# Kernel tuning notes

Hardware: AMD Instinct MI355X
Metric: run time of the kernel (lower is better)

Reference implementation:

```python
import jax, jax.numpy as jnp
import numpy as np

B, L, P, T, D, H = 16, 50, 49, 20, 512, 8
DH = D // H
DFF = 4 * D
EPS = 1e-6
NEG = -1000000000.0


def gelu_tanh(x):
    return 0.5 * x * (1.0 + jnp.tanh(jnp.sqrt(2.0 / jnp.pi) * (x + 0.044715 * x ** 3)))


def layernorm(x, a, b):
    # torch LayerNorm (custom): unbiased std, divide by (std + eps)
    mean = jnp.mean(x, axis=-1, keepdims=True)
    std = jnp.sqrt(jnp.var(x, axis=-1, keepdims=True, ddof=1))
    return a * (x - mean) / (std + EPS) + b


def setup_inputs() -> dict:
    key = jax.random.key(0)
    ks = jax.random.split(key, 20)
    s = 0.02
    return {
        "img": jax.random.normal(ks[0], (B, L, P, D), jnp.float32),
        "title": jax.random.normal(ks[1], (B, L, T, D), jnp.float32),
        "mask": jax.random.randint(ks[2], (B, L, T), 0, 2, jnp.int32),
        "scale_img": jax.random.normal(ks[3], (H, P), jnp.float32) * 0.1,
        "scale_title": jax.random.normal(ks[4], (H, T), jnp.float32) * 0.1,
        "w_proj": jax.random.normal(ks[5], (D, D), jnp.float32) * s,
        "b_proj": jnp.zeros((D,), jnp.float32),
        "w1_img": jax.random.normal(ks[6], (DFF, D), jnp.float32) * s,
        "b1_img": jnp.zeros((DFF,), jnp.float32),
        "w2_img": jax.random.normal(ks[7], (D, DFF), jnp.float32) * s,
        "b2_img": jnp.zeros((D,), jnp.float32),
        "w1_tit": jax.random.normal(ks[8], (DFF, D), jnp.float32) * s,
        "b1_tit": jnp.zeros((DFF,), jnp.float32),
        "w2_tit": jax.random.normal(ks[9], (D, DFF), jnp.float32) * s,
        "b2_tit": jnp.zeros((D,), jnp.float32),
        "ln_a_img": jnp.ones((D,), jnp.float32),
        "ln_b_img": jnp.zeros((D,), jnp.float32),
        "ln_a_tit": jnp.ones((D,), jnp.float32),
        "ln_b_tit": jnp.zeros((D,), jnp.float32),
    }


def _forward(img, title, mask, scale_img, scale_title, w_proj, b_proj,
             w1_img, b1_img, w2_img, b2_img, w1_tit, b1_tit, w2_tit, b2_tit,
             ln_a_img, ln_b_img, ln_a_tit, ln_b_tit):
    imgh = img.reshape(B, L, P, H, DH)      # [B,L,P,H,dh]
    tith = title.reshape(B, L, T, H, DH)    # [B,L,T,H,dh]

    raw = jnp.einsum('blphd,blthd->blhpt', imgh, tith) / jnp.sqrt(jnp.float32(DH))
    # corr_title is the transpose of the UNSCALED corr_img
    corr_img = raw * scale_img[None, None, :, :, None]                     # [B,L,H,P,T]
    corr_tit = jnp.swapaxes(raw, -1, -2) * scale_title[None, None, :, :, None]  # [B,L,H,T,P]

    m_img = mask[:, :, None, None, :]  # [B,L,1,1,T] -> broadcast over H,P
    m_tit = mask[:, :, None, :, None]  # [B,L,1,T,1]
    corr_img = jnp.where(m_img == 0, NEG, corr_img)
    corr_tit = jnp.where(m_tit == 0, NEG, corr_tit)

    p_img = jax.nn.softmax(corr_img, axis=-1)  # [B,L,H,P,T]
    p_tit = jax.nn.softmax(corr_tit, axis=-1)  # [B,L,H,T,P]

    # T != P, so the torch code takes the else branch (swapped outputs)
    hid_img = jnp.einsum('blhtp,blphd->blthd', p_tit, imgh).reshape(B, L, T, D)
    hid_tit = jnp.einsum('blhpt,blthd->blphd', p_img, tith).reshape(B, L, P, D)

    # both projected with img_layer (faithful to source)
    hid_img = hid_img @ w_proj.T + b_proj
    hid_tit = hid_tit @ w_proj.T + b_proj

    ffn_img = gelu_tanh(hid_img @ w1_img.T + b1_img) @ w2_img.T + b2_img
    ffn_tit = gelu_tanh(hid_tit @ w1_tit.T + b1_tit) @ w2_tit.T + b2_tit

    out_img = hid_img + layernorm(ffn_img, ln_a_img, ln_b_img)
    out_tit = hid_tit + layernorm(ffn_tit, ln_a_tit, ln_b_tit)
    return out_img, out_tit


def reference(img, title, mask, scale_img, scale_title, w_proj, b_proj,
              w1_img, b1_img, w2_img, b2_img, w1_tit, b1_tit, w2_tit, b2_tit,
              ln_a_img, ln_b_img, ln_a_tit, ln_b_tit):
    return _forward(img, title, mask, scale_img, scale_title, w_proj, b_proj,
                    w1_img, b1_img, w2_img, b2_img, w1_tit, b1_tit, w2_tit, b2_tit,
                    ln_a_img, ln_b_img, ln_a_tit, ln_b_tit)
```

## Files before the change

### kernel.cpp

```cpp
#include <hip/hip_runtime.h>
#include <hip/hip_bf16.h>

#define BB   16
#define LL   50
#define PP   49
#define TT   20
#define DD   512
#define HH   8
#define DHH  64
#define DFF  2048

#define BL     (BB*LL)
#define ROWS_I (BL*TT)
#define ROWS_T (BL*PP)
#define ROWS_A (ROWS_I+ROWS_T)
#define OUT_I_ELEMS ((size_t)ROWS_I*DD)
#define CHUNK 19600

#define R1_OFF 80281600ull
#define R2_OFF 136806400ull
#define R3_OFF 176947200ull

typedef __attribute__((ext_vector_type(8))) short bf16x8;
typedef __attribute__((ext_vector_type(4))) float f32x4;

__device__ __forceinline__ unsigned short f2bf(float f) {
    union { float f; unsigned int i; } w; w.f = f;
    unsigned int x = w.i;
    unsigned int r = (x + 0x7fffu + ((x >> 16) & 1u)) >> 16;
    return (unsigned short)r;
}
__device__ __forceinline__ float gelu_tanh_f(float x) {
    float c = 0.7978845608028654f * (x + 0.044715f * x * x * x);
    return 0.5f * x * (1.0f + tanhf(c));
}

__global__ __launch_bounds__(256) void cvt_kernel(
    const float* __restrict__ s, unsigned short* __restrict__ d, int n4)
{
    int i = blockIdx.x * 256 + threadIdx.x;
    if (i < n4) {
        float4 v = ((const float4*)s)[i];
        ushort4 u;
        u.x = f2bf(v.x); u.y = f2bf(v.y); u.z = f2bf(v.z); u.w = f2bf(v.w);
        ((ushort4*)d)[i] = u;
    }
}

__global__ __launch_bounds__(256) void attn_kernel(
    const float* __restrict__ img, const float* __restrict__ title,
    const int* __restrict__ mask, const float* __restrict__ scale_img,
    const float* __restrict__ scale_tit, unsigned short* __restrict__ hid)
{
    const int blh = blockIdx.x;
    const int h  = blh & 7;
    const int bl = blh >> 3;
    const int tid = threadIdx.x;

    __shared__ float simg[PP][DHH + 1];
    __shared__ float stit[TT][DHH + 1];
    __shared__ float S [PP][TT];
    __shared__ float pI[PP][TT];
    __shared__ float pT[TT][PP];
    __shared__ int   msk[TT];

    const float* imgbase = img   + (size_t)bl * PP * DD + h * DHH;
    const float* titbase = title + (size_t)bl * TT * DD + h * DHH;
    for (int i = tid; i < PP * DHH; i += 256) {
        int p = i >> 6, d = i & 63;
        simg[p][d] = imgbase[(size_t)p * DD + d];
    }
    for (int i = tid; i < TT * DHH; i += 256) {
        int t = i >> 6, d = i & 63;
        stit[t][d] = titbase[(size_t)t * DD + d];
    }
    if (tid < TT) msk[tid] = mask[bl * TT + tid];
    __syncthreads();

    for (int i = tid; i < PP * TT; i += 256) {
        int p = i / TT, t = i % TT;
        float s = 0.f;
        #pragma unroll 8
        for (int d = 0; d < DHH; ++d) s += simg[p][d] * stit[t][d];
        S[p][t] = s * 0.125f;
    }
    __syncthreads();

    if (tid < PP) {
        const int p = tid;
        const float sc = scale_img[h * PP + p];
        float m = -1e30f;
        #pragma unroll
        for (int t = 0; t < TT; ++t) {
            float x = (msk[t] == 0) ? -1e9f : S[p][t] * sc;
            m = fmaxf(m, x);
        }
        float sum = 0.f;
        #pragma unroll
        for (int t = 0; t < TT; ++t) {
            float x = (msk[t] == 0) ? -1e9f : S[p][t] * sc;
            float e = __expf(x - m);
            pI[p][t] = e; sum += e;
        }
        float inv = 1.f / sum;
        #pragma unroll
        for (int t = 0; t < TT; ++t) pI[p][t] *= inv;
    }
    if (tid >= 64 && tid < 64 + TT) {
        const int t = tid - 64;
        const float sc = scale_tit[h * TT + t];
        const bool dead = (msk[t] == 0);
        float m = -1e30f;
        #pragma unroll
        for (int p = 0; p < PP; ++p) {
            float x = dead ? -1e9f : S[p][t] * sc;
            m = fmaxf(m, x);
        }
        float sum = 0.f;
        #pragma unroll
        for (int p = 0; p < PP; ++p) {
            float x = dead ? -1e9f : S[p][t] * sc;
            float e = __expf(x - m);
            pT[t][p] = e; sum += e;
        }
        float inv = 1.f / sum;
        #pragma unroll
        for (int p = 0; p < PP; ++p) pT[t][p] *= inv;
    }
    __syncthreads();

    for (int i = tid; i < TT * DHH; i += 256) {
        int t = i >> 6, d = i & 63;
        float s = 0.f;
        #pragma unroll
        for (int p = 0; p < PP; ++p) s += pT[t][p] * simg[p][d];
        hid[(size_t)(bl * TT + t) * DD + h * DHH + d] = f2bf(s);
    }
    for (int i = tid; i < PP * DHH; i += 256) {
        int p = i >> 6, d = i & 63;
        float s = 0.f;
        #pragma unroll
        for (int t = 0; t < TT; ++t) s += pI[p][t] * stit[t][d];
        hid[OUT_I_ELEMS + (size_t)(bl * PP + p) * DD + h * DHH + d] = f2bf(s);
    }
}

template<bool GELU, bool F32OUT, bool BF16OUT>
__global__ __launch_bounds__(256) void gemm_mfma(
    const unsigned short* __restrict__ A, const unsigned short* __restrict__ Bw,
    const float* __restrict__ bias,
    float* __restrict__ Cf, unsigned short* __restrict__ Cb,
    int M, int N, int K)
{
    __shared__ unsigned short As[128 * 32];
    __shared__ unsigned short Bs[128 * 32];
    const int tid  = threadIdx.x;
    const int wave = tid >> 6;
    const int lane = tid & 63;
    const int row0 = blockIdx.y * 128;
    const int col0 = blockIdx.x * 128;
    const int m_off = (wave >> 1) * 64;
    const int n_off = (wave & 1) * 64;
    const int lane_m = lane & 15;
    const int lane_k = (lane >> 4) * 8;

    f32x4 acc[4][4] = {};

    for (int k0 = 0; k0 < K; k0 += 32) {
        #pragma unroll
        for (int q = 0; q < 2; ++q) {
            const int li = q * 256 + tid;
            int gr = row0 + (li >> 2);
            if (gr >= M) gr = M - 1;
            const unsigned short* gp = A + (size_t)gr * K + k0 + (li & 3) * 8;
            __builtin_amdgcn_global_load_lds(
                (const __attribute__((address_space(1))) unsigned int*)gp,
                (__attribute__((address_space(3))) unsigned int*)&As[li * 8], 16, 0, 0);
        }
        #pragma unroll
        for (int q = 0; q < 2; ++q) {
            const int li = q * 256 + tid;
            const unsigned short* gp = Bw + (size_t)(col0 + (li >> 2)) * K + k0 + (li & 3) * 8;
            __builtin_amdgcn_global_load_lds(
                (const __attribute__((address_space(1))) unsigned int*)gp,
                (__attribute__((address_space(3))) unsigned int*)&Bs[li * 8], 16, 0, 0);
        }
        __syncthreads();

        bf16x8 af[4], bf[4];
        #pragma unroll
        for (int i = 0; i < 4; ++i) {
            af[i] = *(const bf16x8*)&As[(m_off + i * 16 + lane_m) * 32 + lane_k];
            bf[i] = *(const bf16x8*)&Bs[(n_off + i * 16 + lane_m) * 32 + lane_k];
        }
        #pragma unroll
        for (int i = 0; i < 4; ++i)
            #pragma unroll
            for (int j = 0; j < 4; ++j)
                acc[i][j] = __builtin_amdgcn_mfma_f32_16x16x32_bf16(af[i], bf[j], acc[i][j], 0, 0, 0);
        __syncthreads();
    }

    #pragma unroll
    for (int i = 0; i < 4; ++i) {
        #pragma unroll
        for (int r = 0; r < 4; ++r) {
            const int row = row0 + m_off + i * 16 + (lane >> 4) * 4 + r;
            if (row < M) {
                #pragma unroll
                for (int j = 0; j < 4; ++j) {
                    const int col = col0 + n_off + j * 16 + lane_m;
                    float v = acc[i][j][r] + bias[col];
                    if (GELU) v = gelu_tanh_f(v);
                    if (F32OUT)  Cf[(size_t)row * N + col] = v;
                    if (BF16OUT) Cb[(size_t)row * N + col] = f2bf(v);
                }
            }
        }
    }
}

__global__ __launch_bounds__(256) void ln_res_kernel(
    const float* __restrict__ f2, float* __restrict__ out,
    const float* __restrict__ a, const float* __restrict__ b, int M)
{
    const int wave = threadIdx.x >> 6;
    const int lane = threadIdx.x & 63;
    const int row = blockIdx.x * 4 + wave;
    if (row >= M) return;
    const float* x = f2 + (size_t)row * DD;
    float* o = out + (size_t)row * DD;

    float xs[8];
    float s1 = 0.f, s2 = 0.f;
    #pragma unroll
    for (int i = 0; i < 8; ++i) {
        float v = x[lane + i * 64];
        xs[i] = v; s1 += v; s2 += v * v;
    }
    #pragma unroll
    for (int off = 32; off > 0; off >>= 1) {
        s1 += __shfl_xor(s1, off, 64);
        s2 += __shfl_xor(s2, off, 64);
    }
    const float mean = s1 * (1.f / 512.f);
    float var = (s2 - 512.f * mean * mean) * (1.f / 511.f);
    var = fmaxf(var, 0.f);
    const float rinv = 1.f / (sqrtf(var) + 1e-6f);
    #pragma unroll
    for (int i = 0; i < 8; ++i) {
        const int d = lane + i * 64;
        o[d] = o[d] + a[d] * (xs[i] - mean) * rinv + b[d];
    }
}

extern "C" void kernel_launch(void* const* d_in, const int* in_sizes, int n_in,
                              void* d_out, int out_size, void* d_ws, size_t ws_size,
                              hipStream_t stream) {
    const float* img       = (const float*)d_in[0];
    const float* title     = (const float*)d_in[1];
    const int*   mask      = (const int*)  d_in[2];
    const float* scale_img = (const float*)d_in[3];
    const float* scale_tit = (const float*)d_in[4];
    const float* w_proj    = (const float*)d_in[5];
    const float* b_proj    = (const float*)d_in[6];
    const float* w1_img    = (const float*)d_in[7];
    const float* b1_img    = (const float*)d_in[8];
    const float* w2_img    = (const float*)d_in[9];
    const float* b2_img    = (const float*)d_in[10];
    const float* w1_tit    = (const float*)d_in[11];
    const float* b1_tit    = (const float*)d_in[12];
    const float* w2_tit    = (const float*)d_in[13];
    const float* b2_tit    = (const float*)d_in[14];
    const float* ln_a_img  = (const float*)d_in[15];
    const float* ln_b_img  = (const float*)d_in[16];
    const float* ln_a_tit  = (const float*)d_in[17];
    const float* ln_b_tit  = (const float*)d_in[18];

    float* out = (float*)d_out;
    unsigned short* hid_bf = (unsigned short*)d_ws;
    unsigned short* act    = (unsigned short*)d_ws;
    unsigned short* out_bf = (unsigned short*)((char*)d_ws + R1_OFF);
    float*          f2     = (float*)((char*)d_ws + R2_OFF);
    unsigned short* wp_bf  = (unsigned short*)((char*)d_ws + R3_OFF);
    unsigned short* w1i_bf = wp_bf  + 262144;
    unsigned short* w2i_bf = w1i_bf + 1048576;
    unsigned short* w1t_bf = w2i_bf + 1048576;
    unsigned short* w2t_bf = w1t_bf + 1048576;

    cvt_kernel<<<(262144/4 + 255)/256, 256, 0, stream>>>(w_proj, wp_bf, 262144/4);
    cvt_kernel<<<(1048576/4 + 255)/256, 256, 0, stream>>>(w1_img, w1i_bf, 1048576/4);
    cvt_kernel<<<(1048576/4 + 255)/256, 256, 0, stream>>>(w2_img, w2i_bf, 1048576/4);
    cvt_kernel<<<(1048576/4 + 255)/256, 256, 0, stream>>>(w1_tit, w1t_bf, 1048576/4);
    cvt_kernel<<<(1048576/4 + 255)/256, 256, 0, stream>>>(w2_tit, w2t_bf, 1048576/4);

    attn_kernel<<<BL * HH, 256, 0, stream>>>(img, title, mask, scale_img, scale_tit, hid_bf);

    gemm_mfma<false, true, true><<<dim3(DD/128, (ROWS_A + 127)/128), 256, 0, stream>>>(
        hid_bf, wp_bf, b_proj, out, out_bf, ROWS_A, DD, DD);

    gemm_mfma<true, false, true><<<dim3(DFF/128, (ROWS_I + 127)/128), 256, 0, stream>>>(
        out_bf, w1i_bf, b1_img, nullptr, act, ROWS_I, DFF, DD);
    gemm_mfma<false, true, false><<<dim3(DD/128, (ROWS_I + 127)/128), 256, 0, stream>>>(
        act, w2i_bf, b2_img, f2, nullptr, ROWS_I, DD, DFF);
    ln_res_kernel<<<(ROWS_I + 3)/4, 256, 0, stream>>>(f2, out, ln_a_img, ln_b_img, ROWS_I);

    for (int c = 0; c < 2; ++c) {
        const unsigned short* a1 = out_bf + (size_t)(ROWS_I + c * CHUNK) * DD;
        float* o1 = out + OUT_I_ELEMS + (size_t)c * CHUNK * DD;
        gemm_mfma<true, false, true><<<dim3(DFF/128, (CHUNK + 127)/128), 256, 0, stream>>>(
            a1, w1t_bf, b1_tit, nullptr, act, CHUNK, DFF, DD);
        gemm_mfma<false, true, false><<<dim3(DD/128, (CHUNK + 127)/128), 256, 0, stream>>>(
            act, w2t_bf, b2_tit, f2, nullptr, CHUNK, DD, DFF);
        ln_res_kernel<<<(CHUNK + 3)/4, 256, 0, stream>>>(f2, o1, ln_a_tit, ln_b_tit, CHUNK);
    }
}
```

Before: 946.3 us.

## Use MFMA in attention and bf16 intermediates for FFN output and residual

The attention kernel now stages img/title head slices in LDS as bf16 and computes the score and context products with 16x16x32 bf16 MFMA instructions instead of scalar FP32 loops. The projection GEMM no longer writes an FP32 copy of its output, and the second FFN GEMM writes bf16 instead of FP32. The layernorm-residual kernel reads both bf16 buffers with vectorized loads and writes the final FP32 output once. This cuts FP32 write and read traffic and scalar attention work, at the cost of extra rounding in the residual, FFN output and softmax probabilities.

```diff
diff --git a/kernel.cpp b/kernel.cpp
--- a/kernel.cpp
+++ b/kernel.cpp
@@ -19,11 +19,15 @@
 
 #define R1_OFF 80281600ull
 #define R2_OFF 136806400ull
-#define R3_OFF 176947200ull
+#define R3_OFF 156876800ull
 
 typedef __attribute__((ext_vector_type(8))) short bf16x8;
+typedef __attribute__((ext_vector_type(8))) unsigned short ushort8;
 typedef __attribute__((ext_vector_type(4))) float f32x4;
 
+__device__ __forceinline__ float bf2f(unsigned short u) {
+    union { unsigned int i; float f; } w; w.i = ((unsigned int)u) << 16; return w.f;
+}
 __device__ __forceinline__ unsigned short f2bf(float f) {
     union { float f; unsigned int i; } w; w.f = f;
     unsigned int x = w.i;
@@ -56,100 +60,157 @@
     const int h  = blh & 7;
     const int bl = blh >> 3;
     const int tid = threadIdx.x;
-
-    __shared__ float simg[PP][DHH + 1];
-    __shared__ float stit[TT][DHH + 1];
-    __shared__ float S [PP][TT];
-    __shared__ float pI[PP][TT];
-    __shared__ float pT[TT][PP];
-    __shared__ int   msk[TT];
+    const int w    = tid >> 6;
+    const int lane = tid & 63;
+    const int lane_m = lane & 15;
+    const int lane_q = lane >> 4;
+
+    __shared__ __align__(16) unsigned short s_img [64][72];
+    __shared__ __align__(16) unsigned short s_tit [32][72];
+    __shared__ __align__(16) unsigned short s_imgT[64][72];
+    __shared__ __align__(16) unsigned short s_titT[64][40];
+    __shared__ __align__(16) float          s_S   [64][36];
+    __shared__ __align__(16) unsigned short s_pI  [64][40];
+    __shared__ __align__(16) unsigned short s_pT  [32][72];
+    __shared__ int msk[TT];
 
     const float* imgbase = img   + (size_t)bl * PP * DD + h * DHH;
     const float* titbase = title + (size_t)bl * TT * DD + h * DHH;
-    for (int i = tid; i < PP * DHH; i += 256) {
+
+    for (int i = tid; i < 64 * 64; i += 256) {
         int p = i >> 6, d = i & 63;
-        simg[p][d] = imgbase[(size_t)p * DD + d];
-    }
-    for (int i = tid; i < TT * DHH; i += 256) {
+        s_img[p][d] = (p < PP) ? f2bf(imgbase[(size_t)p * DD + d]) : (unsigned short)0;
+    }
+    for (int i = tid; i < 32 * 64; i += 256) {
         int t = i >> 6, d = i & 63;
-        stit[t][d] = titbase[(size_t)t * DD + d];
+        s_tit[t][d] = (t < TT) ? f2bf(titbase[(size_t)t * DD + d]) : (unsigned short)0;
     }
     if (tid < TT) msk[tid] = mask[bl * TT + tid];
     __syncthreads();
 
-    for (int i = tid; i < PP * TT; i += 256) {
-        int p = i / TT, t = i % TT;
-        float s = 0.f;
-        #pragma unroll 8
-        for (int d = 0; d < DHH; ++d) s += simg[p][d] * stit[t][d];
-        S[p][t] = s * 0.125f;
+    for (int i = tid; i < 64 * 64; i += 256) {
+        int p = i >> 6, d = i & 63;
+        s_imgT[d][p] = s_img[p][d];
+    }
+    for (int i = tid; i < 32 * 64; i += 256) {
+        int t = i >> 6, d = i & 63;
+        s_titT[d][t] = s_tit[t][d];
+    }
+    {
+        f32x4 accS[2] = {};
+        #pragma unroll
+        for (int kk = 0; kk < 2; ++kk) {
+            const int kb = kk * 32 + lane_q * 8;
+            bf16x8 af = *(const bf16x8*)&s_img[w * 16 + lane_m][kb];
+            #pragma unroll
+            for (int nt = 0; nt < 2; ++nt) {
+                bf16x8 bfv = *(const bf16x8*)&s_tit[nt * 16 + lane_m][kb];
+                accS[nt] = __builtin_amdgcn_mfma_f32_16x16x32_bf16(af, bfv, accS[nt], 0, 0, 0);
+            }
+        }
+        #pragma unroll
+        for (int nt = 0; nt < 2; ++nt)
+            #pragma unroll
+            for (int r = 0; r < 4; ++r)
+                s_S[w * 16 + lane_q * 4 + r][nt * 16 + lane_m] = accS[nt][r] * 0.125f;
     }
     __syncthreads();
 
-    if (tid < PP) {
+    if (tid < 64) {
         const int p = tid;
-        const float sc = scale_img[h * PP + p];
-        float m = -1e30f;
-        #pragma unroll
-        for (int t = 0; t < TT; ++t) {
-            float x = (msk[t] == 0) ? -1e9f : S[p][t] * sc;
-            m = fmaxf(m, x);
-        }
-        float sum = 0.f;
-        #pragma unroll
-        for (int t = 0; t < TT; ++t) {
-            float x = (msk[t] == 0) ? -1e9f : S[p][t] * sc;
-            float e = __expf(x - m);
-            pI[p][t] = e; sum += e;
-        }
-        float inv = 1.f / sum;
-        #pragma unroll
-        for (int t = 0; t < TT; ++t) pI[p][t] *= inv;
-    }
-    if (tid >= 64 && tid < 64 + TT) {
+        if (p < PP) {
+            const float sc = scale_img[h * PP + p];
+            float m = -1e30f;
+            #pragma unroll
+            for (int t = 0; t < TT; ++t) {
+                float x = (msk[t] == 0) ? -1e9f : s_S[p][t] * sc;
+                m = fmaxf(m, x);
+            }
+            float e[TT]; float sum = 0.f;
+            #pragma unroll
+            for (int t = 0; t < TT; ++t) {
+                float x = (msk[t] == 0) ? -1e9f : s_S[p][t] * sc;
+                e[t] = __expf(x - m); sum += e[t];
+            }
+            float inv = 1.f / sum;
+            #pragma unroll
+            for (int t = 0; t < TT; ++t) s_pI[p][t] = f2bf(e[t] * inv);
+            for (int t = TT; t < 32; ++t) s_pI[p][t] = 0;
+        } else {
+            for (int t = 0; t < 32; ++t) s_pI[p][t] = 0;
+        }
+    } else if (tid < 96) {
         const int t = tid - 64;
-        const float sc = scale_tit[h * TT + t];
-        const bool dead = (msk[t] == 0);
-        float m = -1e30f;
-        #pragma unroll
-        for (int p = 0; p < PP; ++p) {
-            float x = dead ? -1e9f : S[p][t] * sc;
-            m = fmaxf(m, x);
-        }
-        float sum = 0.f;
-        #pragma unroll
-        for (int p = 0; p < PP; ++p) {
-            float x = dead ? -1e9f : S[p][t] * sc;
-            float e = __expf(x - m);
-            pT[t][p] = e; sum += e;
-        }
-        float inv = 1.f / sum;
-        #pragma unroll
-        for (int p = 0; p < PP; ++p) pT[t][p] *= inv;
+        if (t < TT) {
+            const float sc = scale_tit[h * TT + t];
+            const bool dead = (msk[t] == 0);
+            float m = -1e30f;
+            for (int p = 0; p < PP; ++p) {
+                float x = dead ? -1e9f : s_S[p][t] * sc;
+                m = fmaxf(m, x);
+            }
+            float sum = 0.f;
+            for (int p = 0; p < PP; ++p) {
+                float x = dead ? -1e9f : s_S[p][t] * sc;
+                sum += __expf(x - m);
+            }
+            float inv = 1.f / sum;
+            for (int p = 0; p < PP; ++p) {
+                float x = dead ? -1e9f : s_S[p][t] * sc;
+                s_pT[t][p] = f2bf(__expf(x - m) * inv);
+            }
+            for (int p = PP; p < 64; ++p) s_pT[t][p] = 0;
+        } else {
+            for (int p = 0; p < 64; ++p) s_pT[t][p] = 0;
+        }
     }
     __syncthreads();
 
-    for (int i = tid; i < TT * DHH; i += 256) {
-        int t = i >> 6, d = i & 63;
-        float s = 0.f;
-        #pragma unroll
-        for (int p = 0; p < PP; ++p) s += pT[t][p] * simg[p][d];
-        hid[(size_t)(bl * TT + t) * DD + h * DHH + d] = f2bf(s);
-    }
-    for (int i = tid; i < PP * DHH; i += 256) {
-        int p = i >> 6, d = i & 63;
-        float s = 0.f;
-        #pragma unroll
-        for (int t = 0; t < TT; ++t) s += pI[p][t] * stit[t][d];
-        hid[OUT_I_ELEMS + (size_t)(bl * PP + p) * DD + h * DHH + d] = f2bf(s);
-    }
-}
-
-template<bool GELU, bool F32OUT, bool BF16OUT>
+    {
+        f32x4 acc[2] = {};
+        #pragma unroll
+        for (int kk = 0; kk < 2; ++kk) {
+            const int kb = kk * 32 + lane_q * 8;
+            bf16x8 bfv = *(const bf16x8*)&s_imgT[w * 16 + lane_m][kb];
+            #pragma unroll
+            for (int mt = 0; mt < 2; ++mt) {
+                bf16x8 af = *(const bf16x8*)&s_pT[mt * 16 + lane_m][kb];
+                acc[mt] = __builtin_amdgcn_mfma_f32_16x16x32_bf16(af, bfv, acc[mt], 0, 0, 0);
+            }
+        }
+        #pragma unroll
+        for (int mt = 0; mt < 2; ++mt)
+            #pragma unroll
+            for (int r = 0; r < 4; ++r) {
+                const int t = mt * 16 + lane_q * 4 + r;
+                if (t < TT)
+                    hid[(size_t)(bl * TT + t) * DD + h * DHH + w * 16 + lane_m] = f2bf(acc[mt][r]);
+            }
+    }
+    {
+        f32x4 acc[4] = {};
+        const int kb = lane_q * 8;
+        bf16x8 bfv = *(const bf16x8*)&s_titT[w * 16 + lane_m][kb];
+        #pragma unroll
+        for (int mt = 0; mt < 4; ++mt) {
+            bf16x8 af = *(const bf16x8*)&s_pI[mt * 16 + lane_m][kb];
+            acc[mt] = __builtin_amdgcn_mfma_f32_16x16x32_bf16(af, bfv, acc[mt], 0, 0, 0);
+        }
+        #pragma unroll
+        for (int mt = 0; mt < 4; ++mt)
+            #pragma unroll
+            for (int r = 0; r < 4; ++r) {
+                const int p = mt * 16 + lane_q * 4 + r;
+                if (p < PP)
+                    hid[OUT_I_ELEMS + (size_t)(bl * PP + p) * DD + h * DHH + w * 16 + lane_m] = f2bf(acc[mt][r]);
+            }
+    }
+}
+
+template<bool GELU>
 __global__ __launch_bounds__(256) void gemm_mfma(
     const unsigned short* __restrict__ A, const unsigned short* __restrict__ Bw,
-    const float* __restrict__ bias,
-    float* __restrict__ Cf, unsigned short* __restrict__ Cb,
+    const float* __restrict__ bias, unsigned short* __restrict__ C,
     int M, int N, int K)
 {
     __shared__ unsigned short As[128 * 32];
@@ -187,17 +248,17 @@
         }
         __syncthreads();
 
-        bf16x8 af[4], bf[4];
+        bf16x8 af[4], bfv[4];
         #pragma unroll
         for (int i = 0; i < 4; ++i) {
-            af[i] = *(const bf16x8*)&As[(m_off + i * 16 + lane_m) * 32 + lane_k];
-            bf[i] = *(const bf16x8*)&Bs[(n_off + i * 16 + lane_m) * 32 + lane_k];
+            af[i]  = *(const bf16x8*)&As[(m_off + i * 16 + lane_m) * 32 + lane_k];
+            bfv[i] = *(const bf16x8*)&Bs[(n_off + i * 16 + lane_m) * 32 + lane_k];
         }
         #pragma unroll
         for (int i = 0; i < 4; ++i)
             #pragma unroll
             for (int j = 0; j < 4; ++j)
-                acc[i][j] = __builtin_amdgcn_mfma_f32_16x16x32_bf16(af[i], bf[j], acc[i][j], 0, 0, 0);
+                acc[i][j] = __builtin_amdgcn_mfma_f32_16x16x32_bf16(af[i], bfv[j], acc[i][j], 0, 0, 0);
         __syncthreads();
     }
 
@@ -212,8 +273,7 @@
                     const int col = col0 + n_off + j * 16 + lane_m;
                     float v = acc[i][j][r] + bias[col];
                     if (GELU) v = gelu_tanh_f(v);
-                    if (F32OUT)  Cf[(size_t)row * N + col] = v;
-                    if (BF16OUT) Cb[(size_t)row * N + col] = f2bf(v);
+                    C[(size_t)row * N + col] = f2bf(v);
                 }
             }
         }
@@ -221,22 +281,25 @@
 }
 
 __global__ __launch_bounds__(256) void ln_res_kernel(
-    const float* __restrict__ f2, float* __restrict__ out,
+    const unsigned short* __restrict__ f2, const unsigned short* __restrict__ res,
+    float* __restrict__ out,
     const float* __restrict__ a, const float* __restrict__ b, int M)
 {
     const int wave = threadIdx.x >> 6;
     const int lane = threadIdx.x & 63;
     const int row = blockIdx.x * 4 + wave;
     if (row >= M) return;
-    const float* x = f2 + (size_t)row * DD;
-    float* o = out + (size_t)row * DD;
-
-    float xs[8];
+    const int d0 = lane * 8;
+
+    ushort8 xu = *(const ushort8*)(f2  + (size_t)row * DD + d0);
+    ushort8 ru = *(const ushort8*)(res + (size_t)row * DD + d0);
+    float xs[8], rs[8];
     float s1 = 0.f, s2 = 0.f;
     #pragma unroll
     for (int i = 0; i < 8; ++i) {
-        float v = x[lane + i * 64];
-        xs[i] = v; s1 += v; s2 += v * v;
+        float v = bf2f(xu[i]);
+        xs[i] = v; rs[i] = bf2f(ru[i]);
+        s1 += v; s2 += v * v;
     }
     #pragma unroll
     for (int off = 32; off > 0; off >>= 1) {
@@ -247,11 +310,24 @@
     float var = (s2 - 512.f * mean * mean) * (1.f / 511.f);
     var = fmaxf(var, 0.f);
     const float rinv = 1.f / (sqrtf(var) + 1e-6f);
+
+    float4 a0 = *(const float4*)(a + d0);
+    float4 a1 = *(const float4*)(a + d0 + 4);
+    float4 b0 = *(const float4*)(b + d0);
+    float4 b1 = *(const float4*)(b + d0 + 4);
+    float av[8] = {a0.x,a0.y,a0.z,a0.w,a1.x,a1.y,a1.z,a1.w};
+    float bv[8] = {b0.x,b0.y,b0.z,b0.w,b1.x,b1.y,b1.z,b1.w};
+
+    float4 o0, o1;
+    float ov[8];
     #pragma unroll
-    for (int i = 0; i < 8; ++i) {
-        const int d = lane + i * 64;
-        o[d] = o[d] + a[d] * (xs[i] - mean) * rinv + b[d];
-    }
+    for (int i = 0; i < 8; ++i)
+        ov[i] = rs[i] + av[i] * (xs[i] - mean) * rinv + bv[i];
+    o0.x=ov[0]; o0.y=ov[1]; o0.z=ov[2]; o0.w=ov[3];
+    o1.x=ov[4]; o1.y=ov[5]; o1.z=ov[6]; o1.w=ov[7];
+    float* op = out + (size_t)row * DD + d0;
+    *(float4*)op = o0;
+    *(float4*)(op + 4) = o1;
 }
 
 extern "C" void kernel_launch(void* const* d_in, const int* in_sizes, int n_in,
@@ -281,7 +357,7 @@
     unsigned short* hid_bf = (unsigned short*)d_ws;
     unsigned short* act    = (unsigned short*)d_ws;
     unsigned short* out_bf = (unsigned short*)((char*)d_ws + R1_OFF);
-    float*          f2     = (float*)((char*)d_ws + R2_OFF);
+    unsigned short* f2b    = (unsigned short*)((char*)d_ws + R2_OFF);
     unsigned short* wp_bf  = (unsigned short*)((char*)d_ws + R3_OFF);
     unsigned short* w1i_bf = wp_bf  + 262144;
     unsigned short* w2i_bf = w1i_bf + 1048576;
@@ -296,22 +372,23 @@
 
     attn_kernel<<<BL * HH, 256, 0, stream>>>(img, title, mask, scale_img, scale_tit, hid_bf);
 
-    gemm_mfma<false, true, true><<<dim3(DD/128, (ROWS_A + 127)/128), 256, 0, stream>>>(
-        hid_bf, wp_bf, b_proj, out, out_bf, ROWS_A, DD, DD);
-
-    gemm_mfma<true, false, true><<<dim3(DFF/128, (ROWS_I + 127)/128), 256, 0, stream>>>(
-        out_bf, w1i_bf, b1_img, nullptr, act, ROWS_I, DFF, DD);
-    gemm_mfma<false, true, false><<<dim3(DD/128, (ROWS_I + 127)/128), 256, 0, stream>>>(
-        act, w2i_bf, b2_img, f2, nullptr, ROWS_I, DD, DFF);
-    ln_res_kernel<<<(ROWS_I + 3)/4, 256, 0, stream>>>(f2, out, ln_a_img, ln_b_img, ROWS_I);
+    gemm_mfma<false><<<dim3(DD/128, (ROWS_A + 127)/128), 256, 0, stream>>>(
+        hid_bf, wp_bf, b_proj, out_bf, ROWS_A, DD, DD);
+
+    gemm_mfma<true><<<dim3(DFF/128, (ROWS_I + 127)/128), 256, 0, stream>>>(
+        out_bf, w1i_bf, b1_img, act, ROWS_I, DFF, DD);
+    gemm_mfma<false><<<dim3(DD/128, (ROWS_I + 127)/128), 256, 0, stream>>>(
+        act, w2i_bf, b2_img, f2b, ROWS_I, DD, DFF);
+    ln_res_kernel<<<(ROWS_I + 3)/4, 256, 0, stream>>>(f2b, out_bf, out, ln_a_img, ln_b_img, ROWS_I);
 
     for (int c = 0; c < 2; ++c) {
         const unsigned short* a1 = out_bf + (size_t)(ROWS_I + c * CHUNK) * DD;
         float* o1 = out + OUT_I_ELEMS + (size_t)c * CHUNK * DD;
-        gemm_mfma<true, false, true><<<dim3(DFF/128, (CHUNK + 127)/128), 256, 0, stream>>>(
-            a1, w1t_bf, b1_tit, nullptr, act, CHUNK, DFF, DD);
-        gemm_mfma<false, true, false><<<dim3(DD/128, (CHUNK + 127)/128), 256, 0, stream>>>(
-            act, w2t_bf, b2_tit, f2, nullptr, CHUNK, DD, DFF);
-        ln_res_kernel<<<(CHUNK + 3)/4, 256, 0, stream>>>(f2, o1, ln_a_tit, ln_b_tit, CHUNK);
-    }
-}
+        gemm_mfma<true><<<dim3(DFF/128, (CHUNK + 127)/128), 256, 0, stream>>>(
+            a1, w1t_bf, b1_tit, act, CHUNK, DFF, DD);
+        gemm_mfma<false><<<dim3(DD/128, (CHUNK + 127)/128), 256, 0, stream>>>(
+            act, w2t_bf, b2_tit, f2b, CHUNK, DD, DFF);
+        ln_res_kernel<<<(CHUNK + 3)/4, 256, 0, stream>>>(
+            f2b, out_bf + (size_t)(ROWS_I + c * CHUNK) * DD, o1, ln_a_tit, ln_b_tit, CHUNK);
+    }
+}
```

New measurement: 951.6 us. No clear change (+0.6%).
